# Performance work log

Hardware: AMD Instinct MI355X
Metric: run time of the kernel (lower is better)

The kernel has to match this reference:

```python
import jax, jax.numpy as jnp
from jax import lax
import numpy as np

IN, H, OUT = 14, 28, 2
B, T = 4096, 512


def setup_inputs() -> dict:
    key = jax.random.key(0)
    ks = jax.random.split(key, 7)
    s_ih = 1.0 / np.sqrt(H)
    return {
        "x": jax.random.normal(ks[0], (B, T, IN), dtype=jnp.float32),
        "W_ih": jax.random.uniform(ks[1], (4 * H, IN), jnp.float32, -s_ih, s_ih),
        "W_hh": jax.random.uniform(ks[2], (4 * H, H), jnp.float32, -s_ih, s_ih),
        "b_ih": jax.random.uniform(ks[3], (4 * H,), jnp.float32, -s_ih, s_ih),
        "b_hh": jax.random.uniform(ks[4], (4 * H,), jnp.float32, -s_ih, s_ih),
        "W_out": jax.random.uniform(ks[5], (OUT, H), jnp.float32, -s_ih, s_ih),
        "b_out": jax.random.uniform(ks[6], (OUT,), jnp.float32, -s_ih, s_ih),
    }


def reference(x, W_ih, W_hh, b_ih, b_hh, W_out, b_out):
    # x: [B, T, IN]; PyTorch LSTM gate order: i, f, g, o
    b, h = x.shape[0], W_hh.shape[1]
    h0 = jnp.zeros((b, h), x.dtype)
    c0 = jnp.zeros((b, h), x.dtype)
    # precompute input projection for all timesteps: [T, B, 4H]
    xg = jnp.einsum('bti,gi->tbg', x, W_ih) + b_ih + b_hh

    def step(carry, xt):
        hp, cp = carry
        gates = xt + hp @ W_hh.T            # [B, 4H]
        i, f, g, o = jnp.split(gates, 4, axis=-1)
        c = jax.nn.sigmoid(f) * cp + jax.nn.sigmoid(i) * jnp.tanh(g)
        hn = jax.nn.sigmoid(o) * jnp.tanh(c)
        return (hn, c), None

    (hT, _), _ = lax.scan(step, (h0, c0), xg)
    # out = Linear(r_out[:, -1, :]) == Linear(h_T)
    return hT @ W_out.T + b_out
```

## Files before the change

kernel.cpp:

```cpp
#include <hip/hip_runtime.h>


#define T_STEPS 512
#define BATCH   4096
#define IN_F    14
#define HID     28
#define OUT_N   2
#define MB      16
#define TC      16
#define NCHUNK  (T_STEPS / TC)
#define HPITCH  40
#define XREGS   ((MB * TC * IN_F) / 256)

typedef __attribute__((ext_vector_type(8))) short  short8;
typedef __attribute__((ext_vector_type(4))) float  float4v;

#define L1 1.4426950408889634f
#define L2 2.8853900817779268f

__device__ __forceinline__ unsigned short f2bf(float f) {
    union { float f; unsigned int u; } v; v.f = f;
    unsigned int r = (v.u + 0x7FFFu + ((v.u >> 16) & 1u)) >> 16;
    return (unsigned short)r;
}

__device__ __forceinline__ int cvtpk_bf16(float lo, float hi) {
    int r;
    asm("v_cvt_pk_bf16_f32 %0, %1, %2" : "=v"(r) : "v"(lo), "v"(hi));
    return r;
}

__device__ __forceinline__ void gate4(const float4v pr, float& c, float& hf) {
    float ei = __builtin_amdgcn_exp2f(pr[0] * (-L1));
    float ef = __builtin_amdgcn_exp2f(pr[1] * (-L1));
    float eg = __builtin_amdgcn_exp2f(pr[2] * (-L2));
    float eo = __builtin_amdgcn_exp2f(pr[3] * (-L1));
    float av = 1.0f + ei, bv = 1.0f + ef, dv = 1.0f + eg, vv = 1.0f + eo;
    float pd  = av * dv;
    float pqv = pd * bv;
    float rv  = __builtin_amdgcn_rcpf(pqv);
    float sfv = pd * rv;
    float igv = (1.0f - eg) * bv * rv;
    c = fmaf(sfv, c, igv);
    float ec = __builtin_amdgcn_exp2f(c * (-L2));
    float wv = 1.0f + ec;
    float r2 = __builtin_amdgcn_rcpf(vv * wv);
    hf = (1.0f - ec) * r2;
}

__global__ __launch_bounds__(256, 1)
void lstm_fuse(const float* __restrict__ x,
               const float* __restrict__ W_ih,
               const float* __restrict__ W_hh,
               const float* __restrict__ b_ih,
               const float* __restrict__ b_hh,
               const float* __restrict__ W_out,
               const float* __restrict__ b_out,
               float* __restrict__ out) {
    __shared__ __align__(16) short h_a[2][MB][HPITCH];
    __shared__ __align__(16) short x_a[2][TC][MB][HPITCH];
    __shared__ float hfin[MB][HID];

    const int tid = threadIdx.x;
    const int w   = tid >> 6;
    const int l   = tid & 63;
    const int q   = l >> 4;
    const int m   = l & 15;
    const int b0  = blockIdx.x * MB;

    short8  Ah[2], Ax[2];
    float4v bias[2];
    #pragma unroll
    for (int t = 0; t < 2; ++t) {
        const int ul = 2 * (m >> 2) + t;
        const int ug = 8 * w + ul;
        const bool vr = (ug < HID);
        const int wrow = (m & 3) * HID + (vr ? ug : 0);
        short8 vh, vx;
        #pragma unroll
        for (int j = 0; j < 8; ++j) {
            const int k = 8 * q + j;
            float wh = (vr && k < HID)  ? W_hh[wrow * HID + k]  : 0.0f;
            float wx = (vr && k < IN_F) ? W_ih[wrow * IN_F + k] : 0.0f;
            vh[j] = (short)f2bf(wh);
            vx[j] = (short)f2bf(wx);
        }
        Ah[t] = vh;
        Ax[t] = vx;
        const int u = 8 * w + 2 * q + t;
        float4v bv;
        #pragma unroll
        for (int j = 0; j < 4; ++j)
            bv[j] = (u < HID) ? (b_ih[j * HID + u] + b_hh[j * HID + u]) : 0.0f;
        bias[t] = bv;
    }

    for (int u = tid; u < 2 * MB * HPITCH; u += 256) ((short*)h_a)[u] = 0;
    for (int u = tid; u < 2 * TC * MB * HPITCH; u += 256) ((short*)x_a)[u] = 0;

    const float* xbase = x + (long)b0 * T_STEPS * IN_F;
    float xr[XREGS];
    #pragma unroll
    for (int k = 0; k < XREGS; ++k) {
        const int u  = tid + 256 * k;
        const int bb = u / (TC * IN_F);
        const int r  = u - bb * (TC * IN_F);
        xr[k] = xbase[(long)bb * T_STEPS * IN_F + r];
    }
    __syncthreads();

    const int  ug0 = 8 * w + 2 * q;
    const bool vld = (ug0 < HID);
    float c0 = 0.0f, c1 = 0.0f, h0f = 0.0f, h1f = 0.0f;
    int rb = 0;

    for (int ch = 0; ch < NCHUNK; ++ch) {
        const int buf = ch & 1;
        #pragma unroll
        for (int k = 0; k < XREGS; ++k) {
            const int u  = tid + 256 * k;
            const int bb = u / (TC * IN_F);
            const int r  = u - bb * (TC * IN_F);
            const int t  = r / IN_F;
            const int f  = r - t * IN_F;
            x_a[buf][t][bb][f] = (short)f2bf(xr[k]);
        }
        if (ch + 1 < NCHUNK) {
            #pragma unroll
            for (int k = 0; k < XREGS; ++k) {
                const int u  = tid + 256 * k;
                const int bb = u / (TC * IN_F);
                const int r  = u - bb * (TC * IN_F);
                xr[k] = xbase[(long)bb * T_STEPS * IN_F + (ch + 1) * TC * IN_F + r];
            }
        }
        __syncthreads();

        for (int tt = 0; tt < TC; ++tt) {
            short8 bh = *(const short8*)&h_a[rb][m][8 * q];
            short8 bx = *(const short8*)&x_a[buf][tt][m][8 * q];
            float4v a0 = __builtin_amdgcn_mfma_f32_16x16x32_bf16(Ax[0], bx, bias[0], 0, 0, 0);
            float4v a1 = __builtin_amdgcn_mfma_f32_16x16x32_bf16(Ax[1], bx, bias[1], 0, 0, 0);
            a0 = __builtin_amdgcn_mfma_f32_16x16x32_bf16(Ah[0], bh, a0, 0, 0, 0);
            a1 = __builtin_amdgcn_mfma_f32_16x16x32_bf16(Ah[1], bh, a1, 0, 0, 0);
            if (vld) {
                gate4(a0, c0, h0f);
                gate4(a1, c1, h1f);
                *(int*)&h_a[rb ^ 1][m][ug0] = cvtpk_bf16(h0f, h1f);
            }
            rb ^= 1;
            __syncthreads();
        }
    }

    if (vld) {
        hfin[m][ug0]     = h0f;
        hfin[m][ug0 + 1] = h1f;
    }
    __syncthreads();
    if (tid < MB * OUT_N) {
        const int o  = tid & 1;
        const int bb = tid >> 1;
        float s = b_out[o];
        #pragma unroll
        for (int u = 0; u < HID; ++u)
            s = fmaf(hfin[bb][u], W_out[o * HID + u], s);
        out[(b0 + bb) * OUT_N + o] = s;
    }
}

extern "C" void kernel_launch(void* const* d_in, const int* in_sizes, int n_in,
                              void* d_out, int out_size, void* d_ws, size_t ws_size,
                              hipStream_t stream) {
    const float* x     = (const float*)d_in[0];
    const float* W_ih  = (const float*)d_in[1];
    const float* W_hh  = (const float*)d_in[2];
    const float* b_ih  = (const float*)d_in[3];
    const float* b_hh  = (const float*)d_in[4];
    const float* W_out = (const float*)d_in[5];
    const float* b_out = (const float*)d_in[6];
    float* out = (float*)d_out;

    lstm_fuse<<<BATCH / MB, 256, 0, stream>>>(
        x, W_ih, W_hh, b_ih, b_hh, W_out, b_out, out);
}
```

Before: 285.4 us.

## Split LSTM hidden units across eight waves and prefetch next-step input MFMA

Doubles the block to 512 threads so each of seven active waves handles four hidden units (one MFMA pair per step) instead of four waves handling eight units each. The input-projection MFMA for the next timestep is issued before the gate math of the current step, taking it off the serial recurrence path. This shortens each wave's per-step critical path but makes every barrier cover 512 threads, and one of the eight waves sits idle.

```diff
diff --git a/kernel.cpp b/kernel.cpp
--- a/kernel.cpp
+++ b/kernel.cpp
@@ -10,7 +10,8 @@
 #define TC      16
 #define NCHUNK  (T_STEPS / TC)
 #define HPITCH  40
-#define XREGS   ((MB * TC * IN_F) / 256)
+#define NTHR    512
+#define XREGS   ((MB * TC * IN_F) / NTHR)
 
 typedef __attribute__((ext_vector_type(8))) short  short8;
 typedef __attribute__((ext_vector_type(4))) float  float4v;
@@ -22,12 +23,6 @@
     union { float f; unsigned int u; } v; v.f = f;
     unsigned int r = (v.u + 0x7FFFu + ((v.u >> 16) & 1u)) >> 16;
     return (unsigned short)r;
-}
-
-__device__ __forceinline__ int cvtpk_bf16(float lo, float hi) {
-    int r;
-    asm("v_cvt_pk_bf16_f32 %0, %1, %2" : "=v"(r) : "v"(lo), "v"(hi));
-    return r;
 }
 
 __device__ __forceinline__ void gate4(const float4v pr, float& c, float& hf) {
@@ -48,15 +43,15 @@
     hf = (1.0f - ec) * r2;
 }
 
-__global__ __launch_bounds__(256, 1)
-void lstm_fuse(const float* __restrict__ x,
-               const float* __restrict__ W_ih,
-               const float* __restrict__ W_hh,
-               const float* __restrict__ b_ih,
-               const float* __restrict__ b_hh,
-               const float* __restrict__ W_out,
-               const float* __restrict__ b_out,
-               float* __restrict__ out) {
+__global__ __launch_bounds__(512, 1)
+void lstm_f8(const float* __restrict__ x,
+             const float* __restrict__ W_ih,
+             const float* __restrict__ W_hh,
+             const float* __restrict__ b_ih,
+             const float* __restrict__ b_hh,
+             const float* __restrict__ W_out,
+             const float* __restrict__ b_out,
+             float* __restrict__ out) {
     __shared__ __align__(16) short h_a[2][MB][HPITCH];
     __shared__ __align__(16) short x_a[2][TC][MB][HPITCH];
     __shared__ float hfin[MB][HID];
@@ -67,60 +62,52 @@
     const int q   = l >> 4;
     const int m   = l & 15;
     const int b0  = blockIdx.x * MB;
+    const bool act = (w < 7);
+    const int u   = 4 * w + q;
 
-    short8  Ah[2], Ax[2];
-    float4v bias[2];
-    #pragma unroll
-    for (int t = 0; t < 2; ++t) {
-        const int ul = 2 * (m >> 2) + t;
-        const int ug = 8 * w + ul;
-        const bool vr = (ug < HID);
-        const int wrow = (m & 3) * HID + (vr ? ug : 0);
-        short8 vh, vx;
+    short8  Ah = {0,0,0,0,0,0,0,0}, Ax = {0,0,0,0,0,0,0,0};
+    float4v bias = {0.0f, 0.0f, 0.0f, 0.0f};
+    if (act) {
+        const int unit = 4 * w + (m >> 2);
+        const int wrow = (m & 3) * HID + unit;
         #pragma unroll
         for (int j = 0; j < 8; ++j) {
             const int k = 8 * q + j;
-            float wh = (vr && k < HID)  ? W_hh[wrow * HID + k]  : 0.0f;
-            float wx = (vr && k < IN_F) ? W_ih[wrow * IN_F + k] : 0.0f;
-            vh[j] = (short)f2bf(wh);
-            vx[j] = (short)f2bf(wx);
+            float wh = (k < HID)  ? W_hh[wrow * HID + k]  : 0.0f;
+            float wx = (k < IN_F) ? W_ih[wrow * IN_F + k] : 0.0f;
+            Ah[j] = (short)f2bf(wh);
+            Ax[j] = (short)f2bf(wx);
         }
-        Ah[t] = vh;
-        Ax[t] = vx;
-        const int u = 8 * w + 2 * q + t;
-        float4v bv;
         #pragma unroll
         for (int j = 0; j < 4; ++j)
-            bv[j] = (u < HID) ? (b_ih[j * HID + u] + b_hh[j * HID + u]) : 0.0f;
-        bias[t] = bv;
+            bias[j] = b_ih[j * HID + u] + b_hh[j * HID + u];
     }
 
-    for (int u = tid; u < 2 * MB * HPITCH; u += 256) ((short*)h_a)[u] = 0;
-    for (int u = tid; u < 2 * TC * MB * HPITCH; u += 256) ((short*)x_a)[u] = 0;
+    for (int k = tid; k < 2 * MB * HPITCH; k += NTHR) ((short*)h_a)[k] = 0;
+    for (int k = tid; k < 2 * TC * MB * HPITCH; k += NTHR) ((short*)x_a)[k] = 0;
 
     const float* xbase = x + (long)b0 * T_STEPS * IN_F;
     float xr[XREGS];
     #pragma unroll
     for (int k = 0; k < XREGS; ++k) {
-        const int u  = tid + 256 * k;
-        const int bb = u / (TC * IN_F);
-        const int r  = u - bb * (TC * IN_F);
+        const int u2 = tid + NTHR * k;
+        const int bb = u2 / (TC * IN_F);
+        const int r  = u2 - bb * (TC * IN_F);
         xr[k] = xbase[(long)bb * T_STEPS * IN_F + r];
     }
     __syncthreads();
 
-    const int  ug0 = 8 * w + 2 * q;
-    const bool vld = (ug0 < HID);
-    float c0 = 0.0f, c1 = 0.0f, h0f = 0.0f, h1f = 0.0f;
+    float c = 0.0f, hf = 0.0f;
     int rb = 0;
+    float4v accx = bias;
 
     for (int ch = 0; ch < NCHUNK; ++ch) {
         const int buf = ch & 1;
         #pragma unroll
         for (int k = 0; k < XREGS; ++k) {
-            const int u  = tid + 256 * k;
-            const int bb = u / (TC * IN_F);
-            const int r  = u - bb * (TC * IN_F);
+            const int u2 = tid + NTHR * k;
+            const int bb = u2 / (TC * IN_F);
+            const int r  = u2 - bb * (TC * IN_F);
             const int t  = r / IN_F;
             const int f  = r - t * IN_F;
             x_a[buf][t][bb][f] = (short)f2bf(xr[k]);
@@ -128,43 +115,44 @@
         if (ch + 1 < NCHUNK) {
             #pragma unroll
             for (int k = 0; k < XREGS; ++k) {
-                const int u  = tid + 256 * k;
-                const int bb = u / (TC * IN_F);
-                const int r  = u - bb * (TC * IN_F);
+                const int u2 = tid + NTHR * k;
+                const int bb = u2 / (TC * IN_F);
+                const int r  = u2 - bb * (TC * IN_F);
                 xr[k] = xbase[(long)bb * T_STEPS * IN_F + (ch + 1) * TC * IN_F + r];
             }
         }
         __syncthreads();
 
+        if (act) {
+            short8 bx0 = *(const short8*)&x_a[buf][0][m][8 * q];
+            accx = __builtin_amdgcn_mfma_f32_16x16x32_bf16(Ax, bx0, bias, 0, 0, 0);
+        }
+
         for (int tt = 0; tt < TC; ++tt) {
-            short8 bh = *(const short8*)&h_a[rb][m][8 * q];
-            short8 bx = *(const short8*)&x_a[buf][tt][m][8 * q];
-            float4v a0 = __builtin_amdgcn_mfma_f32_16x16x32_bf16(Ax[0], bx, bias[0], 0, 0, 0);
-            float4v a1 = __builtin_amdgcn_mfma_f32_16x16x32_bf16(Ax[1], bx, bias[1], 0, 0, 0);
-            a0 = __builtin_amdgcn_mfma_f32_16x16x32_bf16(Ah[0], bh, a0, 0, 0, 0);
-            a1 = __builtin_amdgcn_mfma_f32_16x16x32_bf16(Ah[1], bh, a1, 0, 0, 0);
-            if (vld) {
-                gate4(a0, c0, h0f);
-                gate4(a1, c1, h1f);
-                *(int*)&h_a[rb ^ 1][m][ug0] = cvtpk_bf16(h0f, h1f);
+            if (act) {
+                short8 bh = *(const short8*)&h_a[rb][m][8 * q];
+                float4v acc = __builtin_amdgcn_mfma_f32_16x16x32_bf16(Ah, bh, accx, 0, 0, 0);
+                if (tt + 1 < TC) {
+                    short8 bxn = *(const short8*)&x_a[buf][tt + 1][m][8 * q];
+                    accx = __builtin_amdgcn_mfma_f32_16x16x32_bf16(Ax, bxn, bias, 0, 0, 0);
+                }
+                gate4(acc, c, hf);
+                ((short*)&h_a[rb ^ 1][m][0])[u] = (short)f2bf(hf);
             }
             rb ^= 1;
             __syncthreads();
         }
     }
 
-    if (vld) {
-        hfin[m][ug0]     = h0f;
-        hfin[m][ug0 + 1] = h1f;
-    }
+    if (act) hfin[m][u] = hf;
     __syncthreads();
     if (tid < MB * OUT_N) {
         const int o  = tid & 1;
         const int bb = tid >> 1;
         float s = b_out[o];
         #pragma unroll
-        for (int u = 0; u < HID; ++u)
-            s = fmaf(hfin[bb][u], W_out[o * HID + u], s);
+        for (int k = 0; k < HID; ++k)
+            s = fmaf(hfin[bb][k], W_out[o * HID + k], s);
         out[(b0 + bb) * OUT_N + o] = s;
     }
 }
@@ -181,6 +169,6 @@
     const float* b_out = (const float*)d_in[6];
     float* out = (float*)d_out;
 
-    lstm_fuse<<<BATCH / MB, 256, 0, stream>>>(
+    lstm_f8<<<BATCH / MB, NTHR, 0, stream>>>(
         x, W_ih, W_hh, b_ih, b_hh, W_out, b_out, out);
 }
```

After: 273.9 us. 1.04x faster.
